# Optimization experiments

Measured on AMD Instinct MI355X. Metric: run time of the kernel, lower is better.

Reference implementation:

```python
import jax, jax.numpy as jnp
import numpy as np

B, H, W = 2, 64, 64
D = 256  # in_channels
EPS = 1e-5


def conv2d(x, w, pad):
    # x: NCHW, w: OIHW
    return jax.lax.conv_general_dilated(
        x, w, window_strides=(1, 1), padding=[(pad, pad), (pad, pad)],
        dimension_numbers=("NCHW", "OIHW", "NCHW"))


def code_projection(X, codewords, scale):
    # X: [B, D, H, W]; codewords: [K, D]; scale: [D, K]
    b, d = X.shape[0], X.shape[1]
    x = X.reshape(b, d, -1).transpose(0, 2, 1)              # [B, N, D]
    # residual: [B, N, D, K] (large broadcast tensor, as in the original)
    residual = (x[:, :, :, None] - codewords.T[None, None]) * scale
    Q = jax.nn.softmax(-0.5 * jnp.sum(residual ** 2, axis=2), axis=-1)  # [B, N, K]
    Z_num = jnp.einsum("bnk,bndk->bdk", Q, residual)        # sum over N
    Z_ = Z_num / Q.sum(axis=1)[:, None, :]                  # [B, D, K]
    Z = Z_ / jnp.sqrt(jnp.sum(Z_ ** 2, axis=1, keepdims=True))  # L2 over D
    return Z, Q


def graph_conv(inp, weight, gamma, beta):
    # inp: [B, D, K]
    adj = jnp.einsum("bdk,bdl->bkl", inp, inp)              # input^T @ input
    support = jnp.einsum("ij,bjk->bik", weight, inp)        # weight @ input
    out = jnp.einsum("bdk,bkl->bdl", support, adj)          # support @ adj
    out = jax.nn.relu(out)
    # BatchNorm1d (training-mode batch stats over (B, K) per channel D)
    mean = out.mean(axis=(0, 2), keepdims=True)
    var = out.var(axis=(0, 2), keepdims=True)
    return gamma[None, :, None] * (out - mean) / jnp.sqrt(var + EPS) + beta[None, :, None]


def reproj(graph, Q, h, w):
    # graph: [B, D, K], Q: [B, N, K]
    x = jnp.einsum("bdk,bnk->bdn", graph, Q)
    return x.reshape(graph.shape[0], graph.shape[1], h, w)


def branch(c, conv_w, cw, sc, gcnw, g, bta, ext_w, h, w):
    z, q = code_projection(conv2d(c, conv_w, 1), cw, sc)
    z = graph_conv(z, gcnw, g, bta)
    return conv2d(reproj(z, q, h, w), ext_w, 0) + c


def setup_inputs() -> dict:
    key = jax.random.key(0)
    keys = iter(jax.random.split(key, 64))
    nk = lambda: next(keys)
    inp = {}
    inp["c3"] = jax.random.normal(nk(), (B, 512, H, W), jnp.float32)
    inp["c4"] = jax.random.normal(nk(), (B, 512, H, W), jnp.float32)
    inp["c5"] = jax.random.normal(nk(), (B, 512, H, W), jnp.float32)
    for name, K in [("32", 32), ("16", 16), ("8", 8)]:
        inp[f"conv{name}_w"] = jax.random.normal(nk(), (256, 512, 3, 3), jnp.float32) * 0.02
        std1 = 1.0 / np.sqrt(K * D)
        inp[f"cw{name}"] = jax.random.uniform(nk(), (K, D), jnp.float32, -std1, std1)
        inp[f"sc{name}"] = jax.random.uniform(nk(), (D, K), jnp.float32, -1.0, 0.0)
        stdv = 1.0 / np.sqrt(D)
        inp[f"gcnw{name}"] = jax.random.uniform(nk(), (D, D), jnp.float32, -stdv, stdv)
        inp[f"bng{name}"] = jax.random.uniform(nk(), (D,), jnp.float32, 0.5, 1.5)
        inp[f"bnb{name}"] = jax.random.normal(nk(), (D,), jnp.float32) * 0.1
        inp[f"ext{name}_w"] = jax.random.normal(nk(), (512, 256, 1, 1), jnp.float32) * 0.05
    inp["smooth_w"] = jax.random.normal(nk(), (512, 1536, 3, 3), jnp.float32) * 0.01
    inp["smg"] = jax.random.uniform(nk(), (512,), jnp.float32, 0.5, 1.5)
    inp["smb"] = jax.random.normal(nk(), (512,), jnp.float32) * 0.1
    return inp


def reference(c3, c4, c5,
              conv32_w, cw32, sc32, gcnw32, bng32, bnb32, ext32_w,
              conv16_w, cw16, sc16, gcnw16, bng16, bnb16, ext16_w,
              conv8_w, cw8, sc8, gcnw8, bng8, bnb8, ext8_w,
              smooth_w, smg, smb):
    h, w = c3.shape[2], c3.shape[3]
    x_32 = branch(c3, conv32_w, cw32, sc32, gcnw32, bng32, bnb32, ext32_w, h, w)
    x_16 = branch(c4, conv16_w, cw16, sc16, gcnw16, bng16, bnb16, ext16_w, h, w)
    x_8 = branch(c5, conv8_w, cw8, sc8, gcnw8, bng8, bnb8, ext8_w, h, w)
    out = jnp.concatenate([x_8, x_16, x_32], axis=1)        # [B, 1536, H, W]
    out = conv2d(out, smooth_w, 1)
    # BatchNorm2d (training-mode batch stats) + ReLU
    mean = out.mean(axis=(0, 2, 3), keepdims=True)
    var = out.var(axis=(0, 2, 3), keepdims=True)
    out = smg[None, :, None, None] * (out - mean) / jnp.sqrt(var + EPS) + smb[None, :, None, None]
    return jax.nn.relu(out)
```

## Files before the change

### kernel.cpp

```cpp
#include <hip/hip_runtime.h>
#include <hip/hip_bf16.h>
#include <math.h>

#define HWN 4096
#define DCH 256
#define EPSV 1e-5f

typedef unsigned short u16;
typedef __attribute__((ext_vector_type(8))) short short8b;
typedef __attribute__((ext_vector_type(4))) float fx4;
typedef __attribute__((ext_vector_type(8))) unsigned short u16x8;

static __device__ inline u16 f2bf(float f) {
  __hip_bfloat16 h = __float2bfloat16(f);
  return *reinterpret_cast<u16*>(&h);
}
static __device__ inline float bf2f(u16 u) {
  unsigned int v = ((unsigned int)u) << 16;
  return __uint_as_float(v);
}

__global__ __launch_bounds__(256) void t_chwc3_k(const float* __restrict__ i0p,
    const float* __restrict__ i1p, const float* __restrict__ i2p,
    u16* __restrict__ out) {
  __shared__ float tl[32][257];
  const int p0 = blockIdx.x * 256, cic = blockIdx.y;
  const int z = blockIdx.z;
  const int br = z >> 1, b = z & 1;
  const float* in = (br == 0) ? i0p : ((br == 1) ? i1p : i2p);
  const int t = threadIdx.x;
  const float* ip = in + ((size_t)(b * 512 + cic * 32)) * HWN + p0;
#pragma unroll
  for (int r = 0; r < 32; ++r) tl[r][t] = ip[(size_t)r * HWN + t];
  __syncthreads();
  u16* op = out + ((size_t)((z * 16 + cic)) * HWN + p0 + t) * 32;
#pragma unroll
  for (int g = 0; g < 4; ++g) {
    u16x8 o;
#pragma unroll
    for (int j = 0; j < 8; ++j) o[j] = f2bf(tl[g * 8 + j][t]);
    *reinterpret_cast<u16x8*>(op + g * 8) = o;
  }
}

template<int CIN, int COUT>
__global__ __launch_bounds__(256) void wpack_k(const float* __restrict__ w0,
    const float* __restrict__ w1, const float* __restrict__ w2,
    u16* __restrict__ wp) {
  constexpr int NCIC = CIN / 32, NCOG = COUT / 16;
  const int br = blockIdx.y;
  const float* w = (br == 0) ? w0 : ((br == 1) ? w1 : w2);
  u16* wpb = wp + (size_t)br * 9 * NCIC * NCOG * 512;
  const int cog = blockIdx.x % NCOG, cic = blockIdx.x / NCOG;
  __shared__ float ws_[16 * 32 * 9];
  const int t = threadIdx.x;
  const float* src = w + ((size_t)(cog * 16) * CIN + cic * 32) * 9;
  for (int i = t; i < 4608; i += 256) {
    int co = i / 288, r = i % 288;
    ws_[i] = src[(size_t)co * CIN * 9 + r];
  }
  __syncthreads();
  const size_t tapstride = (size_t)NCIC * NCOG * 512;
  const size_t base = ((size_t)cic * NCOG + cog) * 512;
#pragma unroll
  for (int tap = 0; tap < 9; ++tap) {
#pragma unroll
    for (int e0 = 0; e0 < 512; e0 += 256) {
      int e = e0 + t;
      int kg = e >> 7, m = (e >> 3) & 15, j = e & 7;
      wpb[tap * tapstride + base + e] = f2bf(ws_[m * 288 + (kg * 8 + j) * 9 + tap]);
    }
  }
}

template<int CIN, int COUT, int SPLIT, int COW, int WPE, bool BF16OUT>
__global__ __launch_bounds__(256, WPE) void convlds2_k(
    const u16* __restrict__ xt, const u16* __restrict__ wp,
    void* __restrict__ outv) {
  constexpr int NCIC = CIN / 32;
  constexpr int NCO = COUT / COW;
  constexpr int NWT = COW / 16;
  constexpr int CICPS = NCIC / SPLIT;
  constexpr int NST = CICPS * 3;
  constexpr int TAPB = COW * 32;
  constexpr int WSH = TAPB / 4;
  constexpr int RNDS = WSH / 512;
  constexpr int AROW = 66 * 32;
  constexpr size_t OUTEL = (size_t)2 * COUT * HWN;
  __shared__ u16 bl[3 * TAPB];
  __shared__ u16 al[6 * AROW];

  const int br = blockIdx.y;
  xt += (size_t)br * 2 * NCIC * HWN * 32;
  wp += (size_t)br * 9 * NCIC * (COUT / 16) * 512;

  int g = blockIdx.x;
  const int cpx = (int)gridDim.x >> 3;
  g = (g & 7) * cpx + (g >> 3);
  const int s = g / (32 * NCO);
  const int rem = g % (32 * NCO);
  const int rt = rem / NCO;
  const int cob = (rem % NCO) * COW;

  const int wv = threadIdx.x >> 6, lane = threadIdx.x & 63;
  const int b = (rt * 4) >> 6;
  const int h0 = (rt * 4) & 63;
  const int h = h0 + wv;
  const int m = lane & 15, kg = lane >> 4;
  const int cic0 = s * CICPS;
  const int t = threadIdx.x;

  fx4 acc[4][NWT];
#pragma unroll
  for (int i = 0; i < 4; ++i)
#pragma unroll
    for (int jn = 0; jn < NWT; ++jn) acc[i][jn] = (fx4){0.f, 0.f, 0.f, 0.f};

  const u16x8 zero16 = (u16x8){0, 0, 0, 0, 0, 0, 0, 0};
  const int lds_lane = wv * WSH + lane * 8;

  auto stage_a = [&](int cic) {
    const u16* xc = xt + ((size_t)(b * NCIC + cic)) * HWN * 32;
#pragma unroll
    for (int r = 0; r < 6; ++r) {
      const int hl = h0 - 1 + r;
      u16x8 v = zero16;
      if ((unsigned)hl < 64u)
        v = *reinterpret_cast<const u16x8*>(xc + (size_t)hl * 2048 + t * 8);
      *reinterpret_cast<u16x8*>(&al[r * AROW + 32 + t * 8]) = v;
    }
    if (t < 48) {
      int r = t >> 3, side = (t >> 2) & 1, part = t & 3;
      *reinterpret_cast<u16x8*>(&al[r * AROW + (side ? 65 * 32 : 0) + part * 8]) = zero16;
    }
  };

  stage_a(cic0);
  {
#pragma unroll
    for (int t3 = 0; t3 < 3; ++t3) {
      const u16* srcb = wp + (((size_t)t3 * NCIC + cic0) * (COUT / 16) + (cob >> 4)) * 512;
#pragma unroll
      for (int r = 0; r < RNDS; ++r)
        *reinterpret_cast<u16x8*>(&bl[t3 * TAPB + lds_lane + r * 512]) =
            *reinterpret_cast<const u16x8*>(srcb + lds_lane + r * 512);
    }
  }
  __syncthreads();

#pragma unroll 1
  for (int st = 0; st < NST; ++st) {
    const bool hasnext = (st + 1 < NST);
    u16x8 stg[3][RNDS];
    if (hasnext) {
      const int cicn = cic0 + (st + 1) / 3, tyn = (st + 1) % 3;
#pragma unroll
      for (int t3 = 0; t3 < 3; ++t3) {
        const int tap = tyn * 3 + t3;
        const u16* srcb = wp + (((size_t)tap * NCIC + cicn) * (COUT / 16) + (cob >> 4)) * 512;
#pragma unroll
        for (int r = 0; r < RNDS; ++r)
          stg[t3][r] = *reinterpret_cast<const u16x8*>(srcb + lds_lane + r * 512);
      }
    }
    const int ty = st % 3;
    const u16* arow = al + (wv + ty) * AROW + kg * 8;
#pragma unroll
    for (int tx = 0; tx < 3; ++tx) {
      short8b a[4];
#pragma unroll
      for (int mt = 0; mt < 4; ++mt)
        a[mt] = *reinterpret_cast<const short8b*>(arow + (mt * 16 + m + tx) * 32);
      short8b bb[NWT];
#pragma unroll
      for (int nt = 0; nt < NWT; ++nt)
        bb[nt] = *reinterpret_cast<const short8b*>(&bl[tx * TAPB + nt * 512 + lane * 8]);
#pragma unroll
      for (int mt = 0; mt < 4; ++mt)
#pragma unroll
        for (int nt = 0; nt < NWT; ++nt)
          acc[mt][nt] = __builtin_amdgcn_mfma_f32_16x16x32_bf16(a[mt], bb[nt], acc[mt][nt], 0, 0, 0);
    }
    __syncthreads();
    if (hasnext) {
      if (ty == 2) stage_a(cic0 + (st + 1) / 3);
#pragma unroll
      for (int t3 = 0; t3 < 3; ++t3)
#pragma unroll
        for (int r = 0; r < RNDS; ++r)
          *reinterpret_cast<u16x8*>(&bl[t3 * TAPB + lds_lane + r * 512]) = stg[t3][r];
      __syncthreads();
    }
  }

#pragma unroll
  for (int mt = 0; mt < 4; ++mt)
#pragma unroll
    for (int nt = 0; nt < NWT; ++nt) {
      int co = cob + nt * 16 + m;
      size_t idx = ((size_t)(b * COUT + co)) * HWN + h * 64 + mt * 16 + kg * 4;
      if (BF16OUT) {
        u16* op = (u16*)outv + (size_t)(br * SPLIT + s) * OUTEL + idx;
        ushort4 o;
        o.x = f2bf(acc[mt][nt][0]); o.y = f2bf(acc[mt][nt][1]);
        o.z = f2bf(acc[mt][nt][2]); o.w = f2bf(acc[mt][nt][3]);
        *reinterpret_cast<ushort4*>(op) = o;
      } else {
        float* op = (float*)outv + (size_t)(br * SPLIT + s) * OUTEL + idx;
        *reinterpret_cast<fx4*>(op) = acc[mt][nt];
      }
    }
}

__global__ __launch_bounds__(256) void bnall_k(const u16* __restrict__ slab,
    float* __restrict__ dout, const float* __restrict__ gm,
    const float* __restrict__ bt) {
  const int o = blockIdx.x;
  const size_t el = (size_t)2 * 512 * HWN;
  const int t = threadIdx.x;
  float y[2][2][8];
  float s = 0.f, ss = 0.f;
#pragma unroll
  for (int b = 0; b < 2; ++b)
#pragma unroll
    for (int c = 0; c < 2; ++c) {
      const size_t base = ((size_t)(b * 512 + o)) * HWN + c * 2048 + t * 8;
      u16x8 v0 = *reinterpret_cast<const u16x8*>(slab + base);
      u16x8 v1 = *reinterpret_cast<const u16x8*>(slab + el + base);
      u16x8 v2 = *reinterpret_cast<const u16x8*>(slab + 2 * el + base);
      u16x8 v3 = *reinterpret_cast<const u16x8*>(slab + 3 * el + base);
#pragma unroll
      for (int j = 0; j < 8; ++j) {
        float yv = (bf2f(v0[j]) + bf2f(v1[j])) + (bf2f(v2[j]) + bf2f(v3[j]));
        y[b][c][j] = yv; s += yv; ss = fmaf(yv, yv, ss);
      }
    }
  __shared__ float rs[4], rss[4], fin[2];
  for (int off = 32; off; off >>= 1) { s += __shfl_down(s, off); ss += __shfl_down(ss, off); }
  int lane = t & 63, wid = t >> 6;
  if (lane == 0) { rs[wid] = s; rss[wid] = ss; }
  __syncthreads();
  if (t == 0) {
    float S = rs[0] + rs[1] + rs[2] + rs[3];
    float SS = rss[0] + rss[1] + rss[2] + rss[3];
    float mean = S / (2 * HWN);
    float var = SS / (2 * HWN) - mean * mean;
    fin[0] = mean;
    fin[1] = 1.f / sqrtf(var + EPSV);
  }
  __syncthreads();
  const float mean = fin[0], giv = fin[1] * gm[o], be = bt[o];
#pragma unroll
  for (int b = 0; b < 2; ++b)
#pragma unroll
    for (int c = 0; c < 2; ++c) {
      const size_t base = ((size_t)(b * 512 + o)) * HWN + c * 2048 + t * 8;
      fx4 o0, o1;
#pragma unroll
      for (int j = 0; j < 4; ++j)
        o0[j] = fmaxf(fmaf(y[b][c][j] - mean, giv, be), 0.f);
#pragma unroll
      for (int j = 0; j < 4; ++j)
        o1[j] = fmaxf(fmaf(y[b][c][4 + j] - mean, giv, be), 0.f);
      *reinterpret_cast<fx4*>(dout + base) = o0;
      *reinterpret_cast<fx4*>(dout + base + 4) = o1;
    }
}

__global__ __launch_bounds__(256) void prep3_k(
    const float* __restrict__ sc0, const float* __restrict__ sc1, const float* __restrict__ sc2,
    const float* __restrict__ cw0, const float* __restrict__ cw1, const float* __restrict__ cw2,
    float2* __restrict__ AB, float* __restrict__ Ck) {
  const int br = blockIdx.y;
  const int K = 8 << br;
  const int k = blockIdx.x;
  if (k >= K) return;
  const float* sc = (br == 0) ? sc0 : ((br == 1) ? sc1 : sc2);
  const float* cw = (br == 0) ? cw0 : ((br == 1) ? cw1 : cw2);
  float2* ABb = AB + 2048 * ((1 << br) - 1);
  float* Ckb = Ck + 8 * ((1 << br) - 1);
  const int d = threadIdx.x;
  float s = sc[d * K + k];
  float a = s * s;
  float c = cw[k * DCH + d];
  ABb[d * K + k] = make_float2(a, c * a);
  float tt = c * s;
  tt = tt * tt;
  __shared__ float red[4];
  for (int off = 32; off; off >>= 1) tt += __shfl_down(tt, off);
  int lane = threadIdx.x & 63, wid = threadIdx.x >> 6;
  if (lane == 0) red[wid] = tt;
  __syncthreads();
  if (threadIdx.x == 0) Ckb[k] = red[0] + red[1] + red[2] + red[3];
}

template<int K>
static __device__ void score_body(int b, float* sm,
    const u16* __restrict__ s0p, const u16* __restrict__ s1p,
    const float2* __restrict__ AB, const float* __restrict__ Ck,
    float* __restrict__ Qt, float* __restrict__ Qsp) {
  const int lane = threadIdx.x & 63;
  const int g = threadIdx.x >> 6;
  const int n = blockIdx.x * 64 + lane;
  const size_t bbase = ((size_t)b * DCH) * HWN + n;
  float s_[K];
#pragma unroll
  for (int k = 0; k < K; ++k) s_[k] = 0.f;
  for (int d = g * 64; d < g * 64 + 64; ++d) {
    const size_t ofs = bbase + (size_t)d * HWN;
    float xv = bf2f(s0p[ofs]) + bf2f(s1p[ofs]);
    float x2 = xv * xv;
    float xm = -2.f * xv;
    const float2* abp = AB + d * K;
#pragma unroll
    for (int k = 0; k < K; ++k) {
      float2 ab = abp[k];
      s_[k] = fmaf(x2, ab.x, s_[k]);
      s_[k] = fmaf(xm, ab.y, s_[k]);
    }
  }
  float* smr = sm + (g * 64 + lane) * (K + 1);
#pragma unroll
  for (int k = 0; k < K; ++k) smr[k] = s_[k];
  __syncthreads();
  if (g == 0) {
    const float* r0 = sm + lane * (K + 1);
    const float* r1 = sm + (64 + lane) * (K + 1);
    const float* r2 = sm + (128 + lane) * (K + 1);
    const float* r3 = sm + (192 + lane) * (K + 1);
    float mx = -1e30f;
#pragma unroll
    for (int k = 0; k < K; ++k) {
      float v = (r0[k] + r1[k]) + (r2[k] + r3[k]);
      s_[k] = -0.5f * (v + Ck[k]);
      mx = fmaxf(mx, s_[k]);
    }
    float sum = 0.f;
#pragma unroll
    for (int k = 0; k < K; ++k) { float e = expf(s_[k] - mx); s_[k] = e; sum += e; }
    float inv = 1.f / sum;
#pragma unroll
    for (int k = 0; k < K; ++k) {
      float v = s_[k] * inv;
      Qt[((size_t)(b * K + k)) * HWN + n] = v;
      for (int off = 32; off; off >>= 1) v += __shfl_down(v, off);
      if (lane == 0) Qsp[((size_t)(b * K + k)) * 64 + blockIdx.x] = v;
    }
  }
}

__global__ __launch_bounds__(256) void score3_k(const u16* __restrict__ bslab,
    const float2* __restrict__ AB3, const float* __restrict__ Ck3,
    float* __restrict__ Qt3, float* __restrict__ Qsp3) {
  __shared__ float sm[4 * 64 * 33];
  const int z = blockIdx.y, br = z >> 1, b = z & 1;
  const size_t XEL = (size_t)2 * DCH * HWN;
  const u16* s0 = bslab + (size_t)br * 2 * XEL;
  const u16* s1 = s0 + XEL;
  if (br == 0)
    score_body<8>(b, sm, s0, s1, AB3, Ck3, Qt3, Qsp3);
  else if (br == 1)
    score_body<16>(b, sm, s0, s1, AB3 + 2048, Ck3 + 8, Qt3 + 65536, Qsp3 + 1024);
  else
    score_body<32>(b, sm, s0, s1, AB3 + 6144, Ck3 + 24, Qt3 + 196608, Qsp3 + 3072);
}

template<int K>
static __device__ void mmulp_body(int b, float* xs, float* pw,
    const u16* __restrict__ s0p, const u16* __restrict__ s1p,
    const float* __restrict__ Qt, float* __restrict__ Mp) {
  const int d = blockIdx.x, nch = blockIdx.y;
  const int t = threadIdx.x;
  const size_t ofs = ((size_t)(b * DCH + d)) * HWN + nch * 512 + t;
  xs[t] = bf2f(s0p[ofs]) + bf2f(s1p[ofs]);
  xs[t + 256] = bf2f(s0p[ofs + 256]) + bf2f(s1p[ofs + 256]);
  __syncthreads();
  const int lane = t & 63, wid = t >> 6;
#pragma unroll
  for (int k = 0; k < K; ++k) {
    const float* qp = Qt + ((size_t)(b * K + k)) * HWN + nch * 512;
    float s = fmaf(xs[t], qp[t], xs[t + 256] * qp[t + 256]);
    for (int off = 32; off; off >>= 1) s += __shfl_down(s, off);
    if (lane == 0) pw[wid * 33 + k] = s;
  }
  __syncthreads();
  if (t < K)
    Mp[(((size_t)(b * DCH + d)) * K + t) * 8 + nch] =
        (pw[t] + pw[33 + t]) + (pw[66 + t] + pw[99 + t]);
}

__global__ __launch_bounds__(256) void mmulp3_k(const u16* __restrict__ bslab,
    const float* __restrict__ Qt3, float* __restrict__ Mp3) {
  __shared__ float xs[512];
  __shared__ float pw[4 * 33];
  const int z = blockIdx.z, br = z >> 1, b = z & 1;
  const size_t XEL = (size_t)2 * DCH * HWN;
  const u16* s0 = bslab + (size_t)br * 2 * XEL;
  const u16* s1 = s0 + XEL;
  if (br == 0)
    mmulp_body<8>(b, xs, pw, s0, s1, Qt3, Mp3);
  else if (br == 1)
    mmulp_body<16>(b, xs, pw, s0, s1, Qt3 + 65536, Mp3 + 32768);
  else
    mmulp_body<32>(b, xs, pw, s0, s1, Qt3 + 196608, Mp3 + 98304);
}

template<int K>
static __device__ void fuse1_body(int b, float* buf, const float* __restrict__ Mp,
    const float* __restrict__ Qsp, const float* __restrict__ sc,
    const float* __restrict__ cw, const float* __restrict__ Wm,
    float* __restrict__ Graw) {
  float* zl = buf;
  float* adj = zl + DCH * K;
  float* rn = adj + K * K;
  float* qsl = rn + K;
  const int t = threadIdx.x;
  if (t < K) {
    const float* qp = Qsp + ((size_t)(b * K + t)) * 64;
    float s = 0.f;
    for (int i = 0; i < 64; ++i) s += qp[i];
    qsl[t] = s;
  }
  __syncthreads();
#pragma unroll
  for (int k = 0; k < K; ++k) {
    const float* mp = Mp + (((size_t)(b * DCH + t)) * K + k) * 8;
    fx4 p0 = *reinterpret_cast<const fx4*>(mp);
    fx4 p1 = *reinterpret_cast<const fx4*>(mp + 4);
    float mm = ((p0[0] + p0[1]) + (p0[2] + p0[3])) + ((p1[0] + p1[1]) + (p1[2] + p1[3]));
    float qs = qsl[k];
    zl[t * K + k] = sc[t * K + k] * (mm - cw[k * DCH + t] * qs) / qs;
  }
  __syncthreads();
  if (t < K) {
    float s = 0.f;
    for (int i = 0; i < DCH; ++i) { float v = zl[i * K + t]; s = fmaf(v, v, s); }
    rn[t] = 1.f / sqrtf(s);
  }
  __syncthreads();
#pragma unroll
  for (int k = 0; k < K; ++k) zl[t * K + k] *= rn[k];
  __syncthreads();
  for (int p = t; p < K * K; p += 256) {
    int k = p / K, l = p % K;
    float s = 0.f;
    for (int i = 0; i < DCH; ++i) s = fmaf(zl[i * K + k], zl[i * K + l], s);
    adj[p] = s;
  }
  __syncthreads();
  float sup[K];
#pragma unroll
  for (int k = 0; k < K; ++k) sup[k] = 0.f;
  const float* wr = Wm + (size_t)t * DCH;
  for (int jj = 0; jj < DCH; ++jj) {
    float wv = wr[jj];
#pragma unroll
    for (int k = 0; k < K; ++k) sup[k] = fmaf(wv, zl[jj * K + k], sup[k]);
  }
#pragma unroll
  for (int l = 0; l < K; ++l) {
    float s = 0.f;
#pragma unroll
    for (int k = 0; k < K; ++k) s = fmaf(sup[k], adj[k * K + l], s);
    Graw[((size_t)(b * DCH + t)) * K + l] = fmaxf(s, 0.f);
  }
}

__global__ __launch_bounds__(256) void fuse13_k(const float* __restrict__ Mp3,
    const float* __restrict__ Qsp3,
    const float* __restrict__ sc0, const float* __restrict__ sc1, const float* __restrict__ sc2,
    const float* __restrict__ cw0, const float* __restrict__ cw1, const float* __restrict__ cw2,
    const float* __restrict__ wm0, const float* __restrict__ wm1, const float* __restrict__ wm2,
    float* __restrict__ Graw3) {
  __shared__ float buf[DCH * 32 + 32 * 32 + 64];
  const int z = blockIdx.x, br = z >> 1, b = z & 1;
  if (br == 0)
    fuse1_body<8>(b, buf, Mp3, Qsp3, sc0, cw0, wm0, Graw3);
  else if (br == 1)
    fuse1_body<16>(b, buf, Mp3 + 32768, Qsp3 + 1024, sc1, cw1, wm1, Graw3 + 4096);
  else
    fuse1_body<32>(b, buf, Mp3 + 98304, Qsp3 + 3072, sc2, cw2, wm2, Graw3 + 12288);
}

template<int K>
static __device__ void fuse2_body(int b, int ob, float* gl,
    const float* __restrict__ Graw, const float* __restrict__ gamma,
    const float* __restrict__ beta, const float* __restrict__ E,
    float* __restrict__ EG) {
  const int t = threadIdx.x;
  {
    const int d = t;
    float s = 0.f, ss = 0.f;
#pragma unroll
    for (int b2 = 0; b2 < 2; ++b2)
#pragma unroll
      for (int l = 0; l < K; ++l) {
        float v = Graw[((size_t)(b2 * DCH + d)) * K + l];
        s += v; ss = fmaf(v, v, ss);
      }
    const float invn = 1.f / (2 * K);
    float mean = s * invn;
    float var  = ss * invn - mean * mean;
    float giv  = gamma[d] / sqrtf(var + EPSV);
    float be   = beta[d];
#pragma unroll
    for (int l = 0; l < K; ++l) {
      float v = Graw[((size_t)(b * DCH + d)) * K + l];
      gl[d * K + l] = fmaf(v - mean, giv, be);
    }
  }
  __syncthreads();
  const int o = ob * 256 + t;
  float a[K];
#pragma unroll
  for (int k = 0; k < K; ++k) a[k] = 0.f;
  const fx4* e4 = reinterpret_cast<const fx4*>(E + (size_t)o * DCH);
  for (int d4 = 0; d4 < 64; ++d4) {
    fx4 v = e4[d4];
#pragma unroll
    for (int j = 0; j < 4; ++j) {
      float vv = v[j];
#pragma unroll
      for (int k = 0; k < K; ++k)
        a[k] = fmaf(vv, gl[(d4 * 4 + j) * K + k], a[k]);
    }
  }
#pragma unroll
  for (int k = 0; k < K; ++k)
    EG[((size_t)(b * 512 + o)) * K + k] = a[k];
}

__global__ __launch_bounds__(256) void fuse23_k(const float* __restrict__ Graw3,
    const float* __restrict__ g0, const float* __restrict__ g1, const float* __restrict__ g2,
    const float* __restrict__ b0, const float* __restrict__ b1, const float* __restrict__ b2,
    const float* __restrict__ e0, const float* __restrict__ e1, const float* __restrict__ e2,
    float* __restrict__ EG3) {
  __shared__ float gl[DCH * 32];
  const int b = blockIdx.x, ob = blockIdx.y, br = blockIdx.z;
  if (br == 0)
    fuse2_body<8>(b, ob, gl, Graw3, g0, b0, e0, EG3);
  else if (br == 1)
    fuse2_body<16>(b, ob, gl, Graw3 + 4096, g1, b1, e1, EG3 + 8192);
  else
    fuse2_body<32>(b, ob, gl, Graw3 + 12288, g2, b2, e2, EG3 + 24576);
}

template<int K>
static __device__ void yout_body(int b, u16* egl, const float* __restrict__ EG,
    const float* __restrict__ Qt, const float* __restrict__ cres,
    u16* __restrict__ cat, int coff) {
  const int cg = blockIdx.y;
  const int t = threadIdx.x;
  const int lane = t & 63, sub = t >> 6;
  const int n = blockIdx.x * 64 + lane;
  for (int i = t; i < K * 128; i += 256) {
    int k = i >> 7, co = i & 127;
    egl[i] = f2bf(EG[((size_t)(b * 512 + cg * 128 + co)) * K + k]);
  }
  float q[K];
#pragma unroll
  for (int k = 0; k < K; ++k) q[k] = Qt[((size_t)(b * K + k)) * HWN + n];
  __syncthreads();
  const float* crow = cres + (size_t)b * 512 * HWN + n;
#pragma unroll
  for (int it = 0; it < 4; ++it) {
    int co = sub * 32 + it * 8;
    int gco = cg * 128 + co;
    float y[8];
#pragma unroll
    for (int jj = 0; jj < 8; ++jj) y[jj] = crow[(size_t)(gco + jj) * HWN];
#pragma unroll
    for (int k = 0; k < K; ++k) {
      u16x8 eg = *reinterpret_cast<const u16x8*>(&egl[k * 128 + co]);
#pragma unroll
      for (int jj = 0; jj < 8; ++jj) y[jj] = fmaf(bf2f(eg[jj]), q[k], y[jj]);
    }
    u16x8 o;
#pragma unroll
    for (int jj = 0; jj < 8; ++jj) o[jj] = f2bf(y[jj]);
    int ch = coff + gco;
    *reinterpret_cast<u16x8*>(cat +
        (((size_t)(b * 48 + (ch >> 5)) * HWN + n) * 32 + (ch & 31))) = o;
  }
}

__global__ __launch_bounds__(256) void yout3_k(const float* __restrict__ EG3,
    const float* __restrict__ Qt3, const float* __restrict__ c5,
    const float* __restrict__ c4, const float* __restrict__ c3,
    u16* __restrict__ cat) {
  __shared__ u16 egl[32 * 128];
  const int z = blockIdx.z, br = z >> 1, b = z & 1;
  if (br == 0)
    yout_body<8>(b, egl, EG3, Qt3, c5, cat, 0);
  else if (br == 1)
    yout_body<16>(b, egl, EG3 + 8192, Qt3 + 65536, c4, cat, 512);
  else
    yout_body<32>(b, egl, EG3 + 24576, Qt3 + 196608, c3, cat, 1024);
}

extern "C" void kernel_launch(void* const* d_in, const int* in_sizes, int n_in,
                              void* d_out, int out_size, void* d_ws, size_t ws_size,
                              hipStream_t stream) {
  const float* c3 = (const float*)d_in[0];
  const float* c4 = (const float*)d_in[1];
  const float* c5 = (const float*)d_in[2];
  const float* smooth_w = (const float*)d_in[24];
  const float* smg = (const float*)d_in[25];
  const float* smb = (const float*)d_in[26];
  float* dout = (float*)d_out;

  char* wsb = (char*)d_ws;
  u16* Xt3 = (u16*)wsb;
  u16* cat = (u16*)wsb;
  u16* Wb  = (u16*)(wsb + 25165824);
  float* pool  = (float*)(wsb + 39321600);
  char* C = wsb + 43540480;
  u16* bslab   = (u16*)C;
  u16* sslab   = (u16*)C;

  float* Qt3  = pool;
  float* Qsp3 = pool + 458752;
  float* Mp3  = pool + 465920;
  float* Graw3 = pool + 723968;
  float* EG3  = pool + 752640;
  float2* AB3 = (float2*)(pool + 809984);
  float* Ck3  = pool + 838656;

  t_chwc3_k<<<dim3(16, 16, 6), 256, 0, stream>>>(c5, c4, c3, Xt3);
  wpack_k<512, 256><<<dim3(256, 3), 256, 0, stream>>>(
      (const float*)d_in[17], (const float*)d_in[10], (const float*)d_in[3], Wb);
  convlds2_k<512, 256, 2, 64, 3, true><<<dim3(256, 3), 256, 0, stream>>>(Xt3, Wb, bslab);

  prep3_k<<<dim3(32, 3), 256, 0, stream>>>(
      (const float*)d_in[19], (const float*)d_in[12], (const float*)d_in[5],
      (const float*)d_in[18], (const float*)d_in[11], (const float*)d_in[4],
      AB3, Ck3);
  score3_k<<<dim3(64, 6), 256, 0, stream>>>(bslab, AB3, Ck3, Qt3, Qsp3);
  mmulp3_k<<<dim3(256, 8, 6), 256, 0, stream>>>(bslab, Qt3, Mp3);
  fuse13_k<<<6, 256, 0, stream>>>(Mp3, Qsp3,
      (const float*)d_in[19], (const float*)d_in[12], (const float*)d_in[5],
      (const float*)d_in[18], (const float*)d_in[11], (const float*)d_in[4],
      (const float*)d_in[20], (const float*)d_in[13], (const float*)d_in[6],
      Graw3);
  fuse23_k<<<dim3(2, 2, 3), 256, 0, stream>>>(Graw3,
      (const float*)d_in[21], (const float*)d_in[14], (const float*)d_in[7],
      (const float*)d_in[22], (const float*)d_in[15], (const float*)d_in[8],
      (const float*)d_in[23], (const float*)d_in[16], (const float*)d_in[9],
      EG3);
  yout3_k<<<dim3(64, 4, 6), 256, 0, stream>>>(EG3, Qt3, c5, c4, c3, cat);

  wpack_k<1536, 512><<<dim3(1536, 1), 256, 0, stream>>>(smooth_w, smooth_w, smooth_w, Wb);
  convlds2_k<1536, 512, 4, 128, 2, true><<<dim3(512, 1), 256, 0, stream>>>(cat, Wb, sslab);
  bnall_k<<<512, 256, 0, stream>>>(sslab, dout, smg, smb);
}
```

Before: 425.2 us.

## Pad conv input LDS rows and prefetch next input slab into registers

The shared-memory row stride for the input tile grows from 32 to 40 elements per pixel. This is meant to cut LDS bank conflicts on the MFMA A-operand reads. The next channel chunk's input is now loaded from global memory into registers during compute, then written to LDS after the barrier, so that global load latency overlaps with the MFMAs. In exchange it uses more LDS per block and more registers for the staged data, which may lower occupancy.

```diff
diff --git a/kernel.cpp b/kernel.cpp
--- a/kernel.cpp
+++ b/kernel.cpp
@@ -74,7 +74,7 @@
 }
 
 template<int CIN, int COUT, int SPLIT, int COW, int WPE, bool BF16OUT>
-__global__ __launch_bounds__(256, WPE) void convlds2_k(
+__global__ __launch_bounds__(256, WPE) void convlds3_k(
     const u16* __restrict__ xt, const u16* __restrict__ wp,
     void* __restrict__ outv) {
   constexpr int NCIC = CIN / 32;
@@ -85,7 +85,8 @@
   constexpr int TAPB = COW * 32;
   constexpr int WSH = TAPB / 4;
   constexpr int RNDS = WSH / 512;
-  constexpr int AROW = 66 * 32;
+  constexpr int PXS = 40;
+  constexpr int AROW = 66 * PXS;
   constexpr size_t OUTEL = (size_t)2 * COUT * HWN;
   __shared__ u16 bl[3 * TAPB];
   __shared__ u16 al[6 * AROW];
@@ -118,8 +119,10 @@
 
   const u16x8 zero16 = (u16x8){0, 0, 0, 0, 0, 0, 0, 0};
   const int lds_lane = wv * WSH + lane * 8;
-
-  auto stage_a = [&](int cic) {
+  const int a_px = t >> 2, a_sl = t & 3;
+  const int a_wr = (a_px + 1) * PXS + a_sl * 8;
+
+  auto load_a = [&](int cic, u16x8* dst) {
     const u16* xc = xt + ((size_t)(b * NCIC + cic)) * HWN * 32;
 #pragma unroll
     for (int r = 0; r < 6; ++r) {
@@ -127,16 +130,23 @@
       u16x8 v = zero16;
       if ((unsigned)hl < 64u)
         v = *reinterpret_cast<const u16x8*>(xc + (size_t)hl * 2048 + t * 8);
-      *reinterpret_cast<u16x8*>(&al[r * AROW + 32 + t * 8]) = v;
-    }
-    if (t < 48) {
-      int r = t >> 3, side = (t >> 2) & 1, part = t & 3;
-      *reinterpret_cast<u16x8*>(&al[r * AROW + (side ? 65 * 32 : 0) + part * 8]) = zero16;
+      dst[r] = v;
     }
   };
-
-  stage_a(cic0);
+  auto write_a = [&](const u16x8* src) {
+#pragma unroll
+    for (int r = 0; r < 6; ++r)
+      *reinterpret_cast<u16x8*>(&al[r * AROW + a_wr]) = src[r];
+  };
+
+  if (t < 48) {
+    int r = t >> 3, side = (t >> 2) & 1, sl = t & 3;
+    *reinterpret_cast<u16x8*>(&al[r * AROW + (side ? 65 * PXS : 0) + sl * 8]) = zero16;
+  }
   {
+    u16x8 a0[6];
+    load_a(cic0, a0);
+    write_a(a0);
 #pragma unroll
     for (int t3 = 0; t3 < 3; ++t3) {
       const u16* srcb = wp + (((size_t)t3 * NCIC + cic0) * (COUT / 16) + (cob >> 4)) * 512;
@@ -151,7 +161,10 @@
 #pragma unroll 1
   for (int st = 0; st < NST; ++st) {
     const bool hasnext = (st + 1 < NST);
+    const int ty = st % 3;
+    const bool newcic = hasnext && (ty == 2);
     u16x8 stg[3][RNDS];
+    u16x8 astg[6];
     if (hasnext) {
       const int cicn = cic0 + (st + 1) / 3, tyn = (st + 1) % 3;
 #pragma unroll
@@ -162,15 +175,15 @@
         for (int r = 0; r < RNDS; ++r)
           stg[t3][r] = *reinterpret_cast<const u16x8*>(srcb + lds_lane + r * 512);
       }
-    }
-    const int ty = st % 3;
+      if (newcic) load_a(cicn, astg);
+    }
     const u16* arow = al + (wv + ty) * AROW + kg * 8;
 #pragma unroll
     for (int tx = 0; tx < 3; ++tx) {
       short8b a[4];
 #pragma unroll
       for (int mt = 0; mt < 4; ++mt)
-        a[mt] = *reinterpret_cast<const short8b*>(arow + (mt * 16 + m + tx) * 32);
+        a[mt] = *reinterpret_cast<const short8b*>(arow + (mt * 16 + m + tx) * PXS);
       short8b bb[NWT];
 #pragma unroll
       for (int nt = 0; nt < NWT; ++nt)
@@ -183,7 +196,7 @@
     }
     __syncthreads();
     if (hasnext) {
-      if (ty == 2) stage_a(cic0 + (st + 1) / 3);
+      if (newcic) write_a(astg);
 #pragma unroll
       for (int t3 = 0; t3 < 3; ++t3)
 #pragma unroll
@@ -629,7 +642,7 @@
   t_chwc3_k<<<dim3(16, 16, 6), 256, 0, stream>>>(c5, c4, c3, Xt3);
   wpack_k<512, 256><<<dim3(256, 3), 256, 0, stream>>>(
       (const float*)d_in[17], (const float*)d_in[10], (const float*)d_in[3], Wb);
-  convlds2_k<512, 256, 2, 64, 3, true><<<dim3(256, 3), 256, 0, stream>>>(Xt3, Wb, bslab);
+  convlds3_k<512, 256, 2, 64, 3, true><<<dim3(256, 3), 256, 0, stream>>>(Xt3, Wb, bslab);
 
   prep3_k<<<dim3(32, 3), 256, 0, stream>>>(
       (const float*)d_in[19], (const float*)d_in[12], (const float*)d_in[5],
@@ -650,6 +663,6 @@
   yout3_k<<<dim3(64, 4, 6), 256, 0, stream>>>(EG3, Qt3, c5, c4, c3, cat);
 
   wpack_k<1536, 512><<<dim3(1536, 1), 256, 0, stream>>>(smooth_w, smooth_w, smooth_w, Wb);
-  convlds2_k<1536, 512, 4, 128, 2, true><<<dim3(512, 1), 256, 0, stream>>>(cat, Wb, sslab);
+  convlds3_k<1536, 512, 4, 128, 2, true><<<dim3(512, 1), 256, 0, stream>>>(cat, Wb, sslab);
   bnall_k<<<512, 256, 0, stream>>>(sslab, dout, smg, smb);
 }
```

Result: no change. 431.4 us (+1.5%).
